# Performance work log

Hardware: AMD Instinct MI355X
Metric: run time of the kernel (lower is better)

The kernel has to match this reference:

```python
import jax, jax.numpy as jnp
import numpy as np

N_NODES = 100000
N_EDGES = 1600000
IN_DIM = 16
HID = 128
N_LAYERS = 3
LN_EPS = 1e-5


def setup_inputs() -> dict:
    key = jax.random.key(0)
    ks = jax.random.split(key, 8)
    x = jax.random.normal(ks[0], (N_NODES, IN_DIM), dtype=jnp.float32)
    edge_index = jax.random.randint(ks[1], (2, N_EDGES), 0, N_NODES, dtype=jnp.int64)
    # input projection params
    W_in = jax.random.normal(ks[2], (IN_DIM, HID), dtype=jnp.float32) * (1.0 / np.sqrt(IN_DIM))
    b_in = jnp.zeros((HID,), dtype=jnp.float32)
    # stacked GCNConv weights [L, H, H] and biases [L, H]
    W_conv = jax.random.normal(ks[3], (N_LAYERS, HID, HID), dtype=jnp.float32) * (1.0 / np.sqrt(HID))
    b_conv = jnp.zeros((N_LAYERS, HID), dtype=jnp.float32)
    # LayerNorm params [L, H]
    ln_gamma = jnp.ones((N_LAYERS, HID), dtype=jnp.float32)
    ln_beta = jnp.zeros((N_LAYERS, HID), dtype=jnp.float32)
    return {"x": x, "edge_index": edge_index, "W_in": W_in, "b_in": b_in,
            "W_conv": W_conv, "b_conv": b_conv, "ln_gamma": ln_gamma, "ln_beta": ln_beta}


def _layer_norm(h, gamma, beta):
    mu = jnp.mean(h, axis=-1, keepdims=True)
    var = jnp.mean(jnp.square(h - mu), axis=-1, keepdims=True)
    return (h - mu) * jax.lax.rsqrt(var + LN_EPS) * gamma + beta


def reference(x, edge_index, W_in, b_in, W_conv, b_conv, ln_gamma, ln_beta):
    N = x.shape[0]
    loops = jnp.arange(N, dtype=edge_index.dtype)
    src = jnp.concatenate([edge_index[0], loops])  # add self-loops (GCNConv default)
    dst = jnp.concatenate([edge_index[1], loops])
    # symmetric normalization D^-1/2 (A+I) D^-1/2
    deg = jax.ops.segment_sum(jnp.ones(src.shape[0], dtype=x.dtype), dst, num_segments=N)
    dis = jax.lax.rsqrt(jnp.maximum(deg, 1.0))  # deg >= 1 with self-loops
    coef = (dis[src] * dis[dst])[:, None]  # [E+N, 1]
    h = x @ W_in + b_in  # input projection -> [N, HID]
    for l in range(N_LAYERS):
        h_prev = h
        m = h @ W_conv[l]  # transform then propagate (same math as GCNConv)
        agg = jax.ops.segment_sum(m[src] * coef, dst, num_segments=N) + b_conv[l]
        h = jax.nn.relu(_layer_norm(agg, ln_gamma[l], ln_beta[l]))
        if l > 0:  # residual only for i > 0, dims always match
            h = h + h_prev
    return h
```

## Files before the change

### kernel.cpp

```cpp
#include <hip/hip_runtime.h>
#include <hip/hip_bf16.h>
#include <hip/hip_fp16.h>

#define HID 128
#define BCHUNK 4096

typedef __attribute__((ext_vector_type(8))) short short8;
typedef __attribute__((ext_vector_type(4))) float f32x4;

__device__ __forceinline__ float ldf(const void* p, size_t i, int bf16f) {
    if (bf16f) {
        unsigned short u = ((const unsigned short*)p)[i];
        union { unsigned int x; float f; } v; v.x = ((unsigned int)u) << 16;
        return v.f;
    }
    return ((const float*)p)[i];
}
__device__ __forceinline__ int ld_idx(const void* p, size_t i, int i64f) {
    return i64f ? (int)((const long long*)p)[i] : ((const int*)p)[i];
}
__device__ __forceinline__ unsigned short f2bfu(float f) {
    __hip_bfloat16 h = __float2bfloat16(f);
    return *reinterpret_cast<unsigned short*>(&h);
}
__device__ __forceinline__ float bfbits(unsigned int lo16) {
    union { unsigned int x; float f; } v; v.x = lo16 << 16;
    return v.f;
}

__global__ void k_init(const void* __restrict__ gamma, const void* __restrict__ ei,
                       int* flags, int* bkcur, int nbk) {
    int t = threadIdx.x;
    for (int i = t; i < nbk; i += 256) bkcur[i] = 0;
    if (t == 0) {
        unsigned int g0 = ((const unsigned int*)gamma)[0];
        flags[0] = (g0 != 0x3F800000u) ? 1 : 0;
        const unsigned int* e32 = (const unsigned int*)ei;
        int i64 = 1;
        for (int k = 0; k < 128; k++)
            if (e32[2 * k + 1] != 0u) { i64 = 0; break; }
        flags[1] = i64;
    }
}

__global__ __launch_bounds__(256) void k_bucket(const void* __restrict__ ei,
                                                int E, int N, int nbk, int cap,
                                                int* bkcur, unsigned* __restrict__ bdata,
                                                const int* __restrict__ flags) {
    __shared__ int hist[512], base[512];
    int i64 = flags[1];
    int t = threadIdx.x;
    for (int i = t; i < nbk; i += 256) hist[i] = 0;
    __syncthreads();
    int e0 = blockIdx.x * BCHUNK;
    int ss[16], dd[16];
#pragma unroll
    for (int k = 0; k < 16; k++) {
        int e = e0 + k * 256 + t;
        dd[k] = -1;
        if (e < E) {
            int d = ld_idx(ei, (size_t)E + e, i64);
            int s = ld_idx(ei, e, i64);
            if ((unsigned)d < (unsigned)N && (unsigned)s < (unsigned)N) {
                dd[k] = d; ss[k] = s;
                atomicAdd(&hist[d >> 9], 1);
            }
        }
    }
    __syncthreads();
    for (int i = t; i < nbk; i += 256) {
        int c = hist[i];
        base[i] = c ? atomicAdd(&bkcur[i], c) : 0;
        hist[i] = 0;
    }
    __syncthreads();
#pragma unroll
    for (int k = 0; k < 16; k++) {
        if (dd[k] >= 0) {
            int b = dd[k] >> 9;
            int pos = base[b] + atomicAdd(&hist[b], 1);
            if (pos < cap)
                bdata[(size_t)b * cap + pos] =
                    (unsigned)ss[k] | ((unsigned)(dd[k] & 511) << 17);
        }
    }
}

__global__ __launch_bounds__(256) void k_bfused(const int* __restrict__ bkcur,
                                                const unsigned* __restrict__ bdata,
                                                int cap, int* __restrict__ row_ptr,
                                                float* __restrict__ dis,
                                                int* __restrict__ csr_src,
                                                int N, int nbk) {
    __shared__ int hist[512];
    __shared__ int sb[256];
    __shared__ int lsum, bkbase;
    int b = blockIdx.x, t = threadIdx.x;
    int bv = (t < nbk) ? min(bkcur[t], cap) : 0;
    sb[t] = bv;
    __syncthreads();
    int acc = bv;
    for (int off = 1; off < 256; off <<= 1) {
        int x = (t >= off) ? sb[t - off] : 0;
        __syncthreads();
        acc += x; sb[t] = acc;
        __syncthreads();
    }
    if (t == b) bkbase = acc - bv;
    if (b == nbk - 1 && t == nbk - 1) row_ptr[N] = acc;
    for (int i = t; i < 512; i += 256) hist[i] = 0;
    __syncthreads();
    int cb = min(bkcur[b], cap);
    for (int k = t; k < cb; k += 256)
        atomicAdd(&hist[bdata[(size_t)b * cap + k] >> 17], 1);
    __syncthreads();
    int v0 = hist[t], v1 = hist[256 + t];
    int s0 = v0, s1 = v1;
    for (int off = 1; off < 256; off <<= 1) {
        int x0 = (t >= off) ? hist[t - off] : 0;
        int x1 = (t >= off) ? hist[256 + t - off] : 0;
        __syncthreads();
        s0 += x0; s1 += x1;
        hist[t] = s0; hist[256 + t] = s1;
        __syncthreads();
    }
    if (t == 255) lsum = s0;
    __syncthreads();
    int nbase = b << 9;
    int e0 = bkbase + s0 - v0;
    int e1 = bkbase + lsum + s1 - v1;
    if (nbase + t < N) {
        row_ptr[nbase + t] = e0;
        dis[nbase + t] = rsqrtf((float)(v0 + 1));
    }
    if (nbase + 256 + t < N) {
        row_ptr[nbase + 256 + t] = e1;
        dis[nbase + 256 + t] = rsqrtf((float)(v1 + 1));
    }
    __syncthreads();
    hist[t] = e0; hist[256 + t] = e1;
    __syncthreads();
    for (int k = t; k < cb; k += 256) {
        unsigned u = bdata[(size_t)b * cap + k];
        int j = atomicAdd(&hist[u >> 17], 1);
        csr_src[j] = (int)(u & 0x1FFFFu);
    }
}

__global__ void k_proj(const void* __restrict__ x, const void* __restrict__ Win,
                       const void* __restrict__ bin,
                       unsigned short* __restrict__ hb, int N,
                       const void* __restrict__ Wc, unsigned short* __restrict__ Wt,
                       const int* __restrict__ flags) {
    int bf = flags[0];
    int t = threadIdx.x;
    if (blockIdx.x >= N) {
        int i = blockIdx.x - N;
        int l = i >> 7, n = i & 127;
        float w = ldf(Wc, (size_t)l * 16384 + (size_t)t * 128 + n, bf);
        Wt[(size_t)l * 16384 + (size_t)n * 128 + t] = f2bfu(w);
        return;
    }
    int node = blockIdx.x;
    __shared__ float xs[16];
    if (t < 16) xs[t] = ldf(x, (size_t)node * 16 + t, bf);
    __syncthreads();
    float acc = ldf(bin, t, bf);
#pragma unroll
    for (int k = 0; k < 16; k++)
        acc += xs[k] * ldf(Win, (size_t)k * HID + t, bf);
    hb[(size_t)node * HID + t] = f2bfu(acc);
}

__global__ __launch_bounds__(256) void k_gemm(const unsigned short* __restrict__ hb,
                                              const unsigned short* __restrict__ Wt,
                                              unsigned short* __restrict__ m, int N,
                                              int ntiles) {
    int t = threadIdx.x;
    int wave = t >> 6, lane = t & 63;
    int quad = lane >> 4, n15 = lane & 15;
    short8 bfr[4][8];
#pragma unroll
    for (int kc = 0; kc < 4; kc++)
#pragma unroll
        for (int nt = 0; nt < 8; nt++)
            bfr[kc][nt] = *(const short8*)(Wt + (size_t)(nt * 16 + n15) * HID +
                                           kc * 32 + quad * 8);
    int wid = blockIdx.x * 4 + wave;
    int nwaves = gridDim.x * 4;
    for (int tile = wid; tile < ntiles; tile += nwaves) {
        int row0 = tile * 16;
        int arow = min(row0 + n15, N - 1);
        const short8* ap = (const short8*)(hb + (size_t)arow * HID + quad * 8);
        short8 a0 = ap[0], a1 = ap[4], a2 = ap[8], a3 = ap[12];
        f32x4 acc[8] = {};
#pragma unroll
        for (int nt = 0; nt < 8; nt++) {
            acc[nt] = __builtin_amdgcn_mfma_f32_16x16x32_bf16(a0, bfr[0][nt], acc[nt], 0, 0, 0);
            acc[nt] = __builtin_amdgcn_mfma_f32_16x16x32_bf16(a1, bfr[1][nt], acc[nt], 0, 0, 0);
            acc[nt] = __builtin_amdgcn_mfma_f32_16x16x32_bf16(a2, bfr[2][nt], acc[nt], 0, 0, 0);
            acc[nt] = __builtin_amdgcn_mfma_f32_16x16x32_bf16(a3, bfr[3][nt], acc[nt], 0, 0, 0);
        }
#pragma unroll
        for (int nt = 0; nt < 8; nt++)
#pragma unroll
            for (int r = 0; r < 4; r++) {
                int row = row0 + quad * 4 + r;
                if (row < N)
                    m[(size_t)row * HID + nt * 16 + n15] = f2bfu(acc[nt][r]);
            }
    }
}

__global__ __launch_bounds__(256) void k_layer(
        const int* __restrict__ row_ptr, const int* __restrict__ csr_src,
        const unsigned int* __restrict__ m2, const float* __restrict__ dis,
        const void* __restrict__ bc, size_t boff,
        const void* __restrict__ lg, const void* __restrict__ lb, size_t goff,
        unsigned int* __restrict__ hb, void* __restrict__ out, int N,
        int res, int last, const int* __restrict__ flags) {
    int t = threadIdx.x, wave = t >> 6, lane = t & 63;
    int node = blockIdx.x * 4 + wave;
    if (node >= N) return;
    int bf = flags[0];
    float dn = dis[node], dd = dn * dn;
    unsigned int ms = m2[(size_t)node * 64 + lane];
    float v0 = ldf(bc, boff + 2 * lane, bf)     + bfbits(ms & 0xffffu) * dd;
    float v1 = ldf(bc, boff + 2 * lane + 1, bf) + bfbits(ms >> 16) * dd;
    int beg = row_ptr[node], end = row_ptr[node + 1];
    float p0 = 0.f, p1 = 0.f, q0 = 0.f, q1 = 0.f, r0 = 0.f, r1 = 0.f;
    int j = beg;
    for (; j + 3 < end; j += 4) {
        int s0 = csr_src[j], s1 = csr_src[j + 1];
        int s2 = csr_src[j + 2], s3 = csr_src[j + 3];
        float c0 = dis[s0] * dn, c1 = dis[s1] * dn;
        float c2 = dis[s2] * dn, c3 = dis[s3] * dn;
        unsigned int u0 = m2[(size_t)s0 * 64 + lane];
        unsigned int u1 = m2[(size_t)s1 * 64 + lane];
        unsigned int u2 = m2[(size_t)s2 * 64 + lane];
        unsigned int u3 = m2[(size_t)s3 * 64 + lane];
        v0 += bfbits(u0 & 0xffffu) * c0; v1 += bfbits(u0 >> 16) * c0;
        p0 += bfbits(u1 & 0xffffu) * c1; p1 += bfbits(u1 >> 16) * c1;
        q0 += bfbits(u2 & 0xffffu) * c2; q1 += bfbits(u2 >> 16) * c2;
        r0 += bfbits(u3 & 0xffffu) * c3; r1 += bfbits(u3 >> 16) * c3;
    }
    for (; j < end; j++) {
        int s0 = csr_src[j];
        float c0 = dis[s0] * dn;
        unsigned int u0 = m2[(size_t)s0 * 64 + lane];
        v0 += bfbits(u0 & 0xffffu) * c0; v1 += bfbits(u0 >> 16) * c0;
    }
    v0 += p0 + q0 + r0;
    v1 += p1 + q1 + r1;
    float s1 = v0 + v1, s2 = v0 * v0 + v1 * v1;
#pragma unroll
    for (int o = 32; o; o >>= 1) {
        s1 += __shfl_down(s1, o);
        s2 += __shfl_down(s2, o);
    }
    float sum = __shfl(s1, 0), sq = __shfl(s2, 0);
    float mu = sum * (1.0f / HID);
    float var = sq * (1.0f / HID) - mu * mu;
    float r = rsqrtf(var + 1e-5f);
    float g0 = ldf(lg, goff + 2 * lane, bf), g1 = ldf(lg, goff + 2 * lane + 1, bf);
    float b0 = ldf(lb, goff + 2 * lane, bf), b1 = ldf(lb, goff + 2 * lane + 1, bf);
    float o0 = fmaxf((v0 - mu) * r * g0 + b0, 0.f);
    float o1 = fmaxf((v1 - mu) * r * g1 + b1, 0.f);
    size_t widx = (size_t)node * 64 + lane;
    if (res) {
        unsigned int hp = hb[widx];
        o0 += bfbits(hp & 0xffffu);
        o1 += bfbits(hp >> 16);
    }
    unsigned int packed = (unsigned int)f2bfu(o0) | ((unsigned int)f2bfu(o1) << 16);
    hb[widx] = packed;
    if (last) {
        if (bf) ((unsigned int*)out)[widx] = packed;
        else {
            size_t base = (size_t)node * HID + 2 * lane;
            *(float2*)&((float*)out)[base] = make_float2(o0, o1);
        }
    }
}

extern "C" void kernel_launch(void* const* d_in, const int* in_sizes, int n_in,
                              void* d_out, int out_size, void* d_ws, size_t ws_size,
                              hipStream_t stream) {
    const void* x   = d_in[0];
    const void* ei  = d_in[1];
    const void* Win = d_in[2];
    const void* bin = d_in[3];
    const void* Wc  = d_in[4];
    const void* bc  = d_in[5];
    const void* lg  = d_in[6];
    const void* lb  = d_in[7];

    int N = in_sizes[0] / 16;
    int E = in_sizes[1] / 2;
    int nbk = (N + 511) >> 9;
    int cap = ((E / nbk) * 2 + 255) & ~255;

    char* ws = (char*)d_ws;
    size_t off = 0;
    auto alloc = [&](size_t bytes) {
        void* p = ws + off;
        off += (bytes + 255) / 256 * 256;
        return p;
    };
    int*            flags    = (int*)alloc(256);
    float*          dis      = (float*)alloc((size_t)N * 4);
    int*            row_ptr  = (int*)alloc(((size_t)N + 1) * 4);
    int*            bkcur    = (int*)alloc((size_t)nbk * 4);
    unsigned*       bdata    = (unsigned*)alloc((size_t)nbk * cap * 4);
    int*            csr_src  = (int*)alloc((size_t)E * 4);
    unsigned short* hb       = (unsigned short*)alloc((size_t)N * HID * 2);
    unsigned short* m        = (unsigned short*)alloc((size_t)N * HID * 2);
    unsigned short* Wt       = (unsigned short*)alloc((size_t)3 * HID * HID * 2);
    (void)ws_size;

    k_init<<<1, 256, 0, stream>>>(lg, ei, flags, bkcur, nbk);
    k_bucket<<<(E + BCHUNK - 1) / BCHUNK, 256, 0, stream>>>(ei, E, N, nbk, cap,
                                                            bkcur, bdata, flags);
    k_bfused<<<nbk, 256, 0, stream>>>(bkcur, bdata, cap, row_ptr, dis, csr_src,
                                      N, nbk);
    k_proj<<<N + 3 * HID, HID, 0, stream>>>(x, Win, bin, hb, N, Wc, Wt, flags);

    int ntiles = (N + 15) / 16;
    int lblocks = (N + 3) / 4;
    for (int l = 0; l < 3; l++) {
        k_gemm<<<512, 256, 0, stream>>>(hb, Wt + (size_t)l * HID * HID, m, N, ntiles);
        k_layer<<<lblocks, 256, 0, stream>>>(row_ptr, csr_src,
                                             (const unsigned int*)m, dis, bc,
                                             (size_t)l * HID, lg, lb, (size_t)l * HID,
                                             (unsigned int*)hb, d_out, N,
                                             l > 0, l == 2, flags);
    }
}
```

Before: 492.1 us.

## Fold source-side degree scaling into GEMM epilogue and drop per-edge dis gathers

The GEMM epilogue now scales each output row by dis[node], so the gather stage no longer loads dis[src] per edge and applies dn once after summing. The MFMA operands are swapped so each lane holds a row's contiguous columns, letting the epilogue write packed 8-byte stores instead of scattered 2-byte stores. Index math in the gather uses 32-bit unsigned offsets, and the bf16 high-half unpack becomes a mask instead of a shift. The extra rounding of pre-scaled values to bf16 slightly changes numerics.

```diff
diff --git a/kernel.cpp b/kernel.cpp
--- a/kernel.cpp
+++ b/kernel.cpp
@@ -23,8 +23,12 @@
     __hip_bfloat16 h = __float2bfloat16(f);
     return *reinterpret_cast<unsigned short*>(&h);
 }
-__device__ __forceinline__ float bfbits(unsigned int lo16) {
-    union { unsigned int x; float f; } v; v.x = lo16 << 16;
+__device__ __forceinline__ float bflo(unsigned int u) {
+    union { unsigned int x; float f; } v; v.x = u << 16;
+    return v.f;
+}
+__device__ __forceinline__ float bfhi(unsigned int u) {
+    union { unsigned int x; float f; } v; v.x = u & 0xffff0000u;
     return v.f;
 }
 
@@ -174,6 +178,7 @@
 
 __global__ __launch_bounds__(256) void k_gemm(const unsigned short* __restrict__ hb,
                                               const unsigned short* __restrict__ Wt,
+                                              const float* __restrict__ dis,
                                               unsigned short* __restrict__ m, int N,
                                               int ntiles) {
     int t = threadIdx.x;
@@ -190,25 +195,30 @@
     int nwaves = gridDim.x * 4;
     for (int tile = wid; tile < ntiles; tile += nwaves) {
         int row0 = tile * 16;
-        int arow = min(row0 + n15, N - 1);
+        int node = row0 + n15;
+        int arow = min(node, N - 1);
         const short8* ap = (const short8*)(hb + (size_t)arow * HID + quad * 8);
         short8 a0 = ap[0], a1 = ap[4], a2 = ap[8], a3 = ap[12];
+        float dn = dis[arow];
         f32x4 acc[8] = {};
 #pragma unroll
         for (int nt = 0; nt < 8; nt++) {
-            acc[nt] = __builtin_amdgcn_mfma_f32_16x16x32_bf16(a0, bfr[0][nt], acc[nt], 0, 0, 0);
-            acc[nt] = __builtin_amdgcn_mfma_f32_16x16x32_bf16(a1, bfr[1][nt], acc[nt], 0, 0, 0);
-            acc[nt] = __builtin_amdgcn_mfma_f32_16x16x32_bf16(a2, bfr[2][nt], acc[nt], 0, 0, 0);
-            acc[nt] = __builtin_amdgcn_mfma_f32_16x16x32_bf16(a3, bfr[3][nt], acc[nt], 0, 0, 0);
-        }
-#pragma unroll
-        for (int nt = 0; nt < 8; nt++)
-#pragma unroll
-            for (int r = 0; r < 4; r++) {
-                int row = row0 + quad * 4 + r;
-                if (row < N)
-                    m[(size_t)row * HID + nt * 16 + n15] = f2bfu(acc[nt][r]);
+            acc[nt] = __builtin_amdgcn_mfma_f32_16x16x32_bf16(bfr[0][nt], a0, acc[nt], 0, 0, 0);
+            acc[nt] = __builtin_amdgcn_mfma_f32_16x16x32_bf16(bfr[1][nt], a1, acc[nt], 0, 0, 0);
+            acc[nt] = __builtin_amdgcn_mfma_f32_16x16x32_bf16(bfr[2][nt], a2, acc[nt], 0, 0, 0);
+            acc[nt] = __builtin_amdgcn_mfma_f32_16x16x32_bf16(bfr[3][nt], a3, acc[nt], 0, 0, 0);
+        }
+        if (node < N) {
+            unsigned short* mp = m + (size_t)node * HID + quad * 4;
+#pragma unroll
+            for (int nt = 0; nt < 8; nt++) {
+                unsigned lo = (unsigned)f2bfu(acc[nt][0] * dn) |
+                              ((unsigned)f2bfu(acc[nt][1] * dn) << 16);
+                unsigned hi = (unsigned)f2bfu(acc[nt][2] * dn) |
+                              ((unsigned)f2bfu(acc[nt][3] * dn) << 16);
+                *(uint2*)(mp + nt * 16) = make_uint2(lo, hi);
             }
+        }
     }
 }
 
@@ -223,35 +233,33 @@
     int node = blockIdx.x * 4 + wave;
     if (node >= N) return;
     int bf = flags[0];
-    float dn = dis[node], dd = dn * dn;
-    unsigned int ms = m2[(size_t)node * 64 + lane];
-    float v0 = ldf(bc, boff + 2 * lane, bf)     + bfbits(ms & 0xffffu) * dd;
-    float v1 = ldf(bc, boff + 2 * lane + 1, bf) + bfbits(ms >> 16) * dd;
+    float dn = dis[node];
+    unsigned int ms = m2[(unsigned)(node * 64 + lane)];
+    float v0 = bflo(ms), v1 = bfhi(ms);
     int beg = row_ptr[node], end = row_ptr[node + 1];
     float p0 = 0.f, p1 = 0.f, q0 = 0.f, q1 = 0.f, r0 = 0.f, r1 = 0.f;
     int j = beg;
     for (; j + 3 < end; j += 4) {
         int s0 = csr_src[j], s1 = csr_src[j + 1];
         int s2 = csr_src[j + 2], s3 = csr_src[j + 3];
-        float c0 = dis[s0] * dn, c1 = dis[s1] * dn;
-        float c2 = dis[s2] * dn, c3 = dis[s3] * dn;
-        unsigned int u0 = m2[(size_t)s0 * 64 + lane];
-        unsigned int u1 = m2[(size_t)s1 * 64 + lane];
-        unsigned int u2 = m2[(size_t)s2 * 64 + lane];
-        unsigned int u3 = m2[(size_t)s3 * 64 + lane];
-        v0 += bfbits(u0 & 0xffffu) * c0; v1 += bfbits(u0 >> 16) * c0;
-        p0 += bfbits(u1 & 0xffffu) * c1; p1 += bfbits(u1 >> 16) * c1;
-        q0 += bfbits(u2 & 0xffffu) * c2; q1 += bfbits(u2 >> 16) * c2;
-        r0 += bfbits(u3 & 0xffffu) * c3; r1 += bfbits(u3 >> 16) * c3;
+        unsigned int u0 = m2[(unsigned)(s0 * 64 + lane)];
+        unsigned int u1 = m2[(unsigned)(s1 * 64 + lane)];
+        unsigned int u2 = m2[(unsigned)(s2 * 64 + lane)];
+        unsigned int u3 = m2[(unsigned)(s3 * 64 + lane)];
+        v0 += bflo(u0); v1 += bfhi(u0);
+        p0 += bflo(u1); p1 += bfhi(u1);
+        q0 += bflo(u2); q1 += bfhi(u2);
+        r0 += bflo(u3); r1 += bfhi(u3);
     }
     for (; j < end; j++) {
         int s0 = csr_src[j];
-        float c0 = dis[s0] * dn;
-        unsigned int u0 = m2[(size_t)s0 * 64 + lane];
-        v0 += bfbits(u0 & 0xffffu) * c0; v1 += bfbits(u0 >> 16) * c0;
+        unsigned int u0 = m2[(unsigned)(s0 * 64 + lane)];
+        v0 += bflo(u0); v1 += bfhi(u0);
     }
     v0 += p0 + q0 + r0;
     v1 += p1 + q1 + r1;
+    v0 = ldf(bc, boff + 2 * lane, bf) + v0 * dn;
+    v1 = ldf(bc, boff + 2 * lane + 1, bf) + v1 * dn;
     float s1 = v0 + v1, s2 = v0 * v0 + v1 * v1;
 #pragma unroll
     for (int o = 32; o; o >>= 1) {
@@ -269,8 +277,8 @@
     size_t widx = (size_t)node * 64 + lane;
     if (res) {
         unsigned int hp = hb[widx];
-        o0 += bfbits(hp & 0xffffu);
-        o1 += bfbits(hp >> 16);
+        o0 += bflo(hp);
+        o1 += bfhi(hp);
     }
     unsigned int packed = (unsigned int)f2bfu(o0) | ((unsigned int)f2bfu(o1) << 16);
     hb[widx] = packed;
@@ -328,7 +336,8 @@
     int ntiles = (N + 15) / 16;
     int lblocks = (N + 3) / 4;
     for (int l = 0; l < 3; l++) {
-        k_gemm<<<512, 256, 0, stream>>>(hb, Wt + (size_t)l * HID * HID, m, N, ntiles);
+        k_gemm<<<512, 256, 0, stream>>>(hb, Wt + (size_t)l * HID * HID, dis, m, N,
+                                        ntiles);
         k_layer<<<lblocks, 256, 0, stream>>>(row_ptr, csr_src,
                                              (const unsigned int*)m, dis, bc,
                                              (size_t)l * HID, lg, lb, (size_t)l * HID,
```

After: 489.8 us. About the same (-0.5%).
